# Kernel tuning notes

Measured on AMD Instinct MI355X. Metric: run time of the kernel, lower is better.

## Reference

```python
import jax, jax.numpy as jnp
import numpy as np
from jax import lax

N_FRAMES = 256

def _conv(x, w, b):
    # NCHW conv, stride 3 on mel axis (matches MOSNet CNN that collapses mels 81->27->9->3->1)
    y = lax.conv_general_dilated(x, w, window_strides=(1, 3),
                                 padding=((1, 1), (1, 1)),
                                 dimension_numbers=('NCHW', 'OIHW', 'NCHW'))
    return jax.nn.relu(y + b[None, :, None, None])

def _lstm(x, Wih, Whh, bih, bhh, reverse=False):
    # x: [T, B, D] -> hs: [T, B, H]; PyTorch gate order i, f, g, o
    Bsz, H = x.shape[1], Whh.shape[1]
    bias = bih + bhh
    def step(carry, xt):
        h, c = carry
        z = xt @ Wih.T + h @ Whh.T + bias
        i, f, g, o = jnp.split(z, 4, axis=-1)
        c = jax.nn.sigmoid(f) * c + jax.nn.sigmoid(i) * jnp.tanh(g)
        h = jax.nn.sigmoid(o) * jnp.tanh(c)
        return (h, c), h
    init = (jnp.zeros((Bsz, H), x.dtype), jnp.zeros((Bsz, H), x.dtype))
    _, hs = lax.scan(step, init, x, reverse=reverse)
    return hs

def setup_inputs():
    key = jax.random.key(0)
    ks = jax.random.split(key, 24)
    B, T, M = 16, 4096, 81
    chans = [1, 16, 32, 64, 128]
    H = 128
    FC_IN = 2 * H * N_FRAMES  # 65536
    FC_H = 128
    s = 0.05
    inp = {'audio': jax.random.normal(ks[0], (B, T, M), jnp.float32),
           'sample_lengths': jnp.full((B,), T, dtype=jnp.int32)}
    for li in range(4):
        inp['w%d' % li] = jax.random.normal(ks[1 + 2 * li], (chans[li + 1], chans[li], 3, 3), jnp.float32) * s
        inp['b%d' % li] = jnp.zeros((chans[li + 1],), jnp.float32)
    D = chans[-1]
    for d, off in (('f', 9), ('b', 13)):
        inp['Wih_' + d] = jax.random.normal(ks[off], (4 * H, D), jnp.float32) * s
        inp['Whh_' + d] = jax.random.normal(ks[off + 1], (4 * H, H), jnp.float32) * s
        inp['bih_' + d] = jnp.zeros((4 * H,), jnp.float32)
        inp['bhh_' + d] = jnp.zeros((4 * H,), jnp.float32)
    inp['fc1_w'] = jax.random.normal(ks[17], (FC_H, FC_IN), jnp.float32) * 0.005
    inp['fc1_b'] = jnp.zeros((FC_H,), jnp.float32)
    inp['fs_w'] = jax.random.normal(ks[18], (1, FC_H), jnp.float32) * s
    inp['fs_b'] = jnp.zeros((1,), jnp.float32)
    return inp

def reference(audio, w0, b0, w1, b1, w2, b2, w3, b3,
              Wih_f, Whh_f, bih_f, bhh_f, Wih_b, Whh_b, bih_b, bhh_b,
              fc1_w, fc1_b, fs_w, fs_b, sample_lengths):
    B, T, M = audio.shape
    F = T // N_FRAMES  # all lengths == T, multiple of N_FRAMES -> all frames full
    x = audio.reshape(B * F, 1, N_FRAMES, M)   # [BF, 1, nf, mels]
    for w, b in ((w0, b0), (w1, b1), (w2, b2), (w3, b3)):
        x = _conv(x, w, b)                      # mel axis 81->27->9->3->1
    x = x[..., 0].transpose(2, 0, 1)            # [nf, BF, C]
    h_f = _lstm(x, Wih_f, Whh_f, bih_f, bhh_f)
    h_b = _lstm(x, Wih_b, Whh_b, bih_b, bhh_b, reverse=True)
    h = jnp.concatenate([h_f, h_b], axis=-1).transpose(1, 0, 2)  # [BF, nf, 2H]
    flat = h.reshape(B * F, -1)                 # time-major flatten, matches view(1,-1)
    z = jax.nn.relu(flat @ fc1_w.T + fc1_b)     # dropout is identity at inference
    score = jax.nn.sigmoid(z @ fs_w.T + fs_b) * 4.0 + 1.0  # mos range [1,5]
    frames = score.reshape(B, F)
    utt = frames.mean(axis=1)
    return utt, frames
```

## Files before the change

### kernel.cpp

```cpp
#include <hip/hip_runtime.h>
#include <hip/hip_fp16.h>

#define BF 256
#define TSTEPS 256

typedef _Float16 h8_t __attribute__((ext_vector_type(8)));
typedef _Float16 h4_t __attribute__((ext_vector_type(4)));
typedef float f4_t __attribute__((ext_vector_type(4)));

union H8 { uint4 u; h8_t v; };
union H4 { uint2 u; h4_t v; };
union U2H4 { uint2 u; __half h[4]; };

static __device__ __forceinline__ float sigmoidf_(float x) {
    return 1.f / (1.f + __expf(-x));
}
static __device__ __forceinline__ float tanhf_(float x) {
    return 1.f - 2.f / (__expf(2.f * x) + 1.f);
}

static __device__ __forceinline__ void pack_one(const float* __restrict__ src,
                                                __half* __restrict__ dst,
                                                int OC, int IC, int KS,
                                                int oc_str, int ic_str, int k_str, int i) {
    int grp = KS / 4;
    int j = i % grp;
    int oc = (i / grp) % OC;
    int g = (i / (grp * OC)) & 3;
    int chunk = i / (grp * OC * 4);
    int CPK = IC / KS;
    int cc = chunk % CPK;
    int khw = chunk / CPK;
    int ic = cc * KS + g * grp + j;
    dst[i] = __float2half(src[(long)oc * oc_str + (long)ic * ic_str + khw * k_str]);
}

__global__ __launch_bounds__(256) void prep_k(
        const float* __restrict__ w0, const float* __restrict__ w1,
        const float* __restrict__ w2, const float* __restrict__ w3,
        const float* __restrict__ Wihf, const float* __restrict__ Wihb,
        const float* __restrict__ Whhf, const float* __restrict__ Whhb,
        float* __restrict__ w0t, __half* __restrict__ w1p,
        __half* __restrict__ w2p, __half* __restrict__ w3p,
        __half* __restrict__ wfp, __half* __restrict__ wbp,
        __half* __restrict__ whhfp, __half* __restrict__ whhbp) {
    int i = blockIdx.x * 256 + threadIdx.x;
    if (i < 144) { int oc = i / 9, rem = i % 9; w0t[rem * 16 + oc] = w0[i]; return; }
    i -= 144;
    if (i < 4608) { pack_one(w1, w1p, 32, 16, 16, 144, 9, 1, i); return; }
    i -= 4608;
    if (i < 18432) { pack_one(w2, w2p, 64, 32, 32, 288, 9, 1, i); return; }
    i -= 18432;
    if (i < 73728) { pack_one(w3, w3p, 128, 64, 32, 576, 9, 1, i); return; }
    i -= 73728;
    if (i < 65536) { pack_one(Wihf, wfp, 512, 128, 32, 128, 1, 0, i); return; }
    i -= 65536;
    if (i < 65536) { pack_one(Wihb, wbp, 512, 128, 32, 128, 1, 0, i); return; }
    i -= 65536;
    if (i < 65536) { pack_one(Whhf, whhfp, 512, 128, 32, 128, 1, 0, i); return; }
    i -= 65536;
    if (i < 65536) { pack_one(Whhb, whhbp, 512, 128, 32, 128, 1, 0, i); return; }
}

__global__ void pack_wf16(const float* __restrict__ src, __half* __restrict__ dst,
                          int OC, int IC, int KS,
                          int oc_str, int ic_str, int k_str, int total) {
    int i = blockIdx.x * 256 + threadIdx.x;
    if (i >= total) return;
    pack_one(src, dst, OC, IC, KS, oc_str, ic_str, k_str, i);
}

__global__ __launch_bounds__(256) void conv0_k(const float* __restrict__ in,
                                               const float* __restrict__ wT,
                                               const float* __restrict__ bias,
                                               __half* __restrict__ out) {
    __shared__ float wsm[9][16];
    __shared__ float bs[16];
    int tid = threadIdx.x;
    if (tid < 144) wsm[tid / 16][tid % 16] = wT[tid];
    if (tid < 16) bs[tid] = bias[tid];
    __syncthreads();
    int gid = blockIdx.x * 256 + tid;
    int ow = gid % 27;
    int t = (gid / 27) % 256;
    int bf = gid / (27 * 256);
    float acc[16];
#pragma unroll
    for (int o = 0; o < 16; o++) acc[o] = bs[o];
    int iw0 = ow * 3 - 1;
#pragma unroll
    for (int kh = 0; kh < 3; kh++) {
        int tt = t + kh - 1;
        if ((unsigned)tt >= 256u) continue;
        const float* ip = in + ((long)bf * 256 + tt) * 81;
#pragma unroll
        for (int kw = 0; kw < 3; kw++) {
            int iw = iw0 + kw;
            if ((unsigned)iw >= 81u) continue;
            float x = ip[iw];
#pragma unroll
            for (int o = 0; o < 16; o++) acc[o] += x * wsm[kh * 3 + kw][o];
        }
    }
    __half2* op = (__half2*)(out + (long)gid * 16);
#pragma unroll
    for (int o = 0; o < 8; o++)
        op[o] = __floats2half2_rn(fmaxf(acc[2 * o], 0.f), fmaxf(acc[2 * o + 1], 0.f));
}

template<int IC, int OC, int WIN, int WOUT, int KS>
__global__ __launch_bounds__(256) void convM_k(const __half* __restrict__ in,
                                               const __half* __restrict__ wp,
                                               const float* __restrict__ bias,
                                               __half* __restrict__ out) {
    constexpr int NT = OC / 16;
    constexpr int CPK = IC / KS;
    constexpr int NCHUNK = 9 * CPK;
    constexpr int GRP = KS / 4;
    int tid = threadIdx.x;
    int lane = tid & 63;
    int wv = tid >> 6;
    int l15 = lane & 15;
    int g = lane >> 4;
    int m = blockIdx.x * 64 + wv * 16 + l15;
    int ow = m % WOUT;
    int t = (m / WOUT) % 256;
    int bf = m / (WOUT * 256);

    f4_t acc[NT];
#pragma unroll
    for (int nt = 0; nt < NT; nt++)
#pragma unroll
        for (int r = 0; r < 4; r++) acc[nt][r] = 0.f;

#pragma unroll
    for (int chunk = 0; chunk < NCHUNK; chunk++) {
        int khw = chunk / CPK, cc = chunk % CPK;
        int kh = khw / 3;
        int kw = khw - kh * 3;
        int tt = t + kh - 1;
        int iw = ow * 3 + kw - 1;
        bool ok = ((unsigned)tt < 256u) && ((unsigned)iw < (unsigned)WIN);
        long aoff = ok ? (((long)(bf * 256 + tt) * WIN + iw) * IC + cc * KS + g * GRP) : 0;
        if constexpr (KS == 32) {
            H8 af;
            af.u = *(const uint4*)(in + aoff);
            if (!ok) af.u = make_uint4(0u, 0u, 0u, 0u);
#pragma unroll
            for (int nt = 0; nt < NT; nt++) {
                H8 bf8;
                bf8.u = *(const uint4*)(wp + ((long)(chunk * 4 + g) * OC + nt * 16 + l15) * GRP);
                acc[nt] = __builtin_amdgcn_mfma_f32_16x16x32_f16(af.v, bf8.v, acc[nt], 0, 0, 0);
            }
        } else {
            H4 af;
            af.u = *(const uint2*)(in + aoff);
            if (!ok) af.u = make_uint2(0u, 0u);
#pragma unroll
            for (int nt = 0; nt < NT; nt++) {
                H4 bf4;
                bf4.u = *(const uint2*)(wp + ((long)(chunk * 4 + g) * OC + nt * 16 + l15) * GRP);
                acc[nt] = __builtin_amdgcn_mfma_f32_16x16x16f16(af.v, bf4.v, acc[nt], 0, 0, 0);
            }
        }
    }
    int orow = blockIdx.x * 64 + wv * 16 + g * 4;
#pragma unroll
    for (int nt = 0; nt < NT; nt++) {
        int oc = nt * 16 + l15;
        float b = bias[oc];
#pragma unroll
        for (int r = 0; r < 4; r++) {
            float v = fmaxf(acc[nt][r] + b, 0.f);
            out[(long)(orow + r) * OC + oc] = __float2half(v);
        }
    }
}

__global__ __launch_bounds__(256) void gates_k(const __half* __restrict__ X,
                                               const __half* __restrict__ wpf,
                                               const __half* __restrict__ wpb,
                                               const float* __restrict__ bf1,
                                               const float* __restrict__ bf2,
                                               const float* __restrict__ bb1,
                                               const float* __restrict__ bb2,
                                               __half* __restrict__ Gf,
                                               __half* __restrict__ Gb) {
    int dir = blockIdx.z;
    const __half* wp = dir ? wpb : wpf;
    const float* b1 = dir ? bb1 : bf1;
    const float* b2 = dir ? bb2 : bf2;
    __half* G = dir ? Gb : Gf;
    int tid = threadIdx.x;
    int lane = tid & 63;
    int wv = tid >> 6;
    int l15 = lane & 15;
    int g = lane >> 4;
    long r0 = (long)blockIdx.x * 128 + wv * 32;
    int n0 = blockIdx.y * 128;

    f4_t acc[2][8];
#pragma unroll
    for (int s = 0; s < 2; s++)
#pragma unroll
        for (int nt = 0; nt < 8; nt++)
#pragma unroll
            for (int r = 0; r < 4; r++) acc[s][nt][r] = 0.f;

#pragma unroll
    for (int chunk = 0; chunk < 4; chunk++) {
        H8 a0, a1;
        a0.u = *(const uint4*)(X + (r0 + l15) * 128 + chunk * 32 + g * 8);
        a1.u = *(const uint4*)(X + (r0 + 16 + l15) * 128 + chunk * 32 + g * 8);
#pragma unroll
        for (int nt = 0; nt < 8; nt++) {
            H8 bw;
            bw.u = *(const uint4*)(wp + ((long)(chunk * 4 + g) * 512 + n0 + nt * 16 + l15) * 8);
            acc[0][nt] = __builtin_amdgcn_mfma_f32_16x16x32_f16(a0.v, bw.v, acc[0][nt], 0, 0, 0);
            acc[1][nt] = __builtin_amdgcn_mfma_f32_16x16x32_f16(a1.v, bw.v, acc[1][nt], 0, 0, 0);
        }
    }
    int b = (int)(r0 >> 8);
#pragma unroll
    for (int nt = 0; nt < 8; nt++) {
        int col = n0 + nt * 16 + l15;
        float bias = b1[col] + b2[col];
        long base = ((long)b * 512 + col) * 256;
#pragma unroll
        for (int s = 0; s < 2; s++) {
            int tb = (int)(r0 & 255) + s * 16 + g * 4;
            U2H4 pk;
            if (!dir) {
#pragma unroll
                for (int r = 0; r < 4; r++) pk.h[r] = __float2half(acc[s][nt][r] + bias);
                *(uint2*)(G + base + tb) = pk.u;
            } else {
#pragma unroll
                for (int r = 0; r < 4; r++) pk.h[3 - r] = __float2half(acc[s][nt][r] + bias);
                *(uint2*)(G + base + (252 - tb)) = pk.u;
            }
        }
    }
}

__global__ __launch_bounds__(512, 2) void lstm_k(const __half* __restrict__ Gf,
                                                 const __half* __restrict__ Gb,
                                                 const __half* __restrict__ whhfp,
                                                 const __half* __restrict__ whhbp,
                                                 __half* __restrict__ flat) {
    int bid = blockIdx.x;
    int dir = bid >> 7;
    int b0 = (bid & 127) * 2;
    const __half* G = dir ? Gb : Gf;
    const __half* wp = dir ? whhbp : whhfp;
    int tid = threadIdx.x;
    int w = tid >> 6;
    int lane = tid & 63;
    int l15 = lane & 15;
    int g2 = lane >> 4;
    int chn = l15 >> 3;
    int r = l15 & 3;
    int bit2 = (l15 >> 2) & 1;
    int ua = w * 16 + g2 * 4 + r;
    bool wrt = bit2 && ((r & 1) == 0);

    H8 afr[4][4];
#pragma unroll
    for (int k = 0; k < 4; k++) {
        int gate = k * 128 + w * 16 + l15;
#pragma unroll
        for (int c = 0; c < 4; c++)
            afr[k][c].u = *(const uint4*)(wp + ((long)((c * 4 + g2) * 512 + gate)) * 8);
    }

    __shared__ __align__(16) __half hbuf[2][2][128];
    if (tid < 256) hbuf[0][tid >> 7][tid & 127] = __float2half(0.f);
    __syncthreads();

    const __half* gb0 = G + (((long)(b0 + chn) * 512) + bit2 * 256 + ua) * 256;
    const __half* gb1 = gb0 + 128 * 256;

    float cst = 0.f;
    float ma = bit2 ? 2.f : 1.f;
    float mb = bit2 ? 2.f : 1.f;
    float cb = bit2 ? -1.f : 0.f;
    const f4_t zero4 = {0.f, 0.f, 0.f, 0.f};

    H8 gc0, gc1, gn0, gn1;
    gc0.u = *(const uint4*)(gb0);
    gc1.u = *(const uint4*)(gb1);
    long fbase = (long)(b0 + chn) * 65536 + dir * 128 + ua;

    for (int to = 0; to < 32; to++) {
        if (to < 31) {
            gn0.u = *(const uint4*)(gb0 + (to + 1) * 8);
            gn1.u = *(const uint4*)(gb1 + (to + 1) * 8);
        }
#pragma unroll
        for (int ti = 0; ti < 8; ti++) {
            int s = to * 8 + ti;
            int p = s & 1;
            H8 bfr[4];
#pragma unroll
            for (int c = 0; c < 4; c++)
                bfr[c].u = *(const uint4*)(&hbuf[p][chn][c * 32 + g2 * 8]);

            f4_t acc[4];
#pragma unroll
            for (int k = 0; k < 4; k++)
                acc[k] = __builtin_amdgcn_mfma_f32_16x16x32_f16(afr[k][0].v, bfr[0].v,
                                                                zero4, 0, 0, 0);
#pragma unroll
            for (int c = 1; c < 4; c++)
#pragma unroll
                for (int k = 0; k < 4; k++)
                    acc[k] = __builtin_amdgcn_mfma_f32_16x16x32_f16(afr[k][c].v, bfr[c].v,
                                                                    acc[k], 0, 0, 0);
            f4_t aA, aB;
#pragma unroll
            for (int e = 0; e < 4; e++) {
                aA[e] = bit2 ? acc[2][e] : acc[0][e];
                aB[e] = bit2 ? acc[3][e] : acc[1][e];
            }
            float loA = (r & 1) ? aA[1] : aA[0];
            float hiA = (r & 1) ? aA[3] : aA[2];
            float eA = (r & 2) ? hiA : loA;
            float loB = (r & 1) ? aB[1] : aB[0];
            float hiB = (r & 1) ? aB[3] : aB[2];
            float eB = (r & 2) ? hiB : loB;

            float za = eA + (float)gc0.v[ti];
            float zb = eB + (float)gc1.v[ti];
            float sa = sigmoidf_(ma * za);
            float fa = sa * mb + cb;
            float sb = sigmoidf_(zb);
            float grecv = __shfl_xor(fa, 4, 64);
            float cn = sb * cst + fa * grecv;
            cst = cn;
            float tc = tanhf_(cn);
            float tcr = __shfl_xor(tc, 4, 64);
            float h = sb * tcr;
            float hp = __shfl_xor(h, 1, 64);
            if (wrt) {
                __half2 h2 = __floats2half2_rn(h, hp);
                int ts = dir ? (255 - s) : s;
                *(__half2*)(&hbuf[p ^ 1][chn][ua]) = h2;
                *(__half2*)(flat + fbase + (long)ts * 256) = h2;
            }
            __syncthreads();
        }
        gc0 = gn0;
        gc1 = gn1;
    }
}

__global__ __launch_bounds__(256) void fc1m_k(const __half* __restrict__ flat,
                                              const __half* __restrict__ wp,
                                              float* __restrict__ z) {
    int tid = threadIdx.x;
    int lane = tid & 63;
    int wv = tid >> 6;
    int l15 = lane & 15;
    int g = lane >> 4;
    int m0 = blockIdx.x * 64 + wv * 16;
    long k0 = (long)blockIdx.y * 1024;

    f4_t acc[8];
#pragma unroll
    for (int nt = 0; nt < 8; nt++)
#pragma unroll
        for (int r = 0; r < 4; r++) acc[nt][r] = 0.f;

    for (int c = 0; c < 32; c++) {
        long chunk = (k0 >> 5) + c;
        H8 af;
        af.u = *(const uint4*)(flat + (long)(m0 + l15) * 65536 + k0 + c * 32 + g * 8);
#pragma unroll
        for (int nt = 0; nt < 8; nt++) {
            H8 bw;
            bw.u = *(const uint4*)(wp + ((chunk * 4 + g) * 128 + nt * 16 + l15) * 8);
            acc[nt] = __builtin_amdgcn_mfma_f32_16x16x32_f16(af.v, bw.v, acc[nt], 0, 0, 0);
        }
    }
#pragma unroll
    for (int nt = 0; nt < 8; nt++)
#pragma unroll
        for (int r = 0; r < 4; r++)
            atomicAdd(&z[(m0 + g * 4 + r) * 128 + nt * 16 + l15], acc[nt][r]);
}

__global__ void zero_k(float* __restrict__ p, int n) {
    int i = blockIdx.x * 256 + threadIdx.x;
    if (i < n) p[i] = 0.f;
}

__global__ __launch_bounds__(256) void head_k(const float* __restrict__ z,
                                              const float* __restrict__ b1,
                                              const float* __restrict__ fsw,
                                              const float* __restrict__ fsb,
                                              float* __restrict__ out) {
    __shared__ float sf[256];
    int r = threadIdx.x;
    float acc = fsb[0];
#pragma unroll
    for (int j4 = 0; j4 < 32; j4++) {
        float4 zv = *(const float4*)&z[r * 128 + j4 * 4];
        float4 bv = *(const float4*)&b1[j4 * 4];
        float4 wv = *(const float4*)&fsw[j4 * 4];
        acc += fmaxf(zv.x + bv.x, 0.f) * wv.x;
        acc += fmaxf(zv.y + bv.y, 0.f) * wv.y;
        acc += fmaxf(zv.z + bv.z, 0.f) * wv.z;
        acc += fmaxf(zv.w + bv.w, 0.f) * wv.w;
    }
    float val = sigmoidf_(acc) * 4.f + 1.f;
    out[16 + r] = val;
    sf[r] = val;
    __syncthreads();
    if (r < 16) {
        float m = 0.f;
#pragma unroll
        for (int f = 0; f < 16; f++) m += sf[r * 16 + f];
        out[r] = m * (1.f / 16.f);
    }
}

extern "C" void kernel_launch(void* const* d_in, const int* in_sizes, int n_in,
                              void* d_out, int out_size, void* d_ws, size_t ws_size,
                              hipStream_t stream) {
    const float* audio = (const float*)d_in[0];
    const float* w0 = (const float*)d_in[2];
    const float* b0 = (const float*)d_in[3];
    const float* w1 = (const float*)d_in[4];
    const float* b1 = (const float*)d_in[5];
    const float* w2 = (const float*)d_in[6];
    const float* b2 = (const float*)d_in[7];
    const float* w3 = (const float*)d_in[8];
    const float* b3 = (const float*)d_in[9];
    const float* Wih_f = (const float*)d_in[10];
    const float* Whh_f = (const float*)d_in[11];
    const float* bih_f = (const float*)d_in[12];
    const float* bhh_f = (const float*)d_in[13];
    const float* Wih_b = (const float*)d_in[14];
    const float* Whh_b = (const float*)d_in[15];
    const float* bih_b = (const float*)d_in[16];
    const float* bhh_b = (const float*)d_in[17];
    const float* fc1_w = (const float*)d_in[18];
    const float* fc1_b = (const float*)d_in[19];
    const float* fs_w = (const float*)d_in[20];
    const float* fs_b = (const float*)d_in[21];
    float* out = (float*)d_out;

    char* ws = (char*)d_ws;
    __half* Gf    = (__half*)(ws);
    __half* out1  = (__half*)(ws);
    __half* fc1p  = (__half*)(ws);
    __half* Gb    = (__half*)(ws + 67108864);
    __half* flat16= (__half*)(ws + 134217728);
    __half* out0  = (__half*)(ws + 134217728);
    __half* X     = (__half*)(ws + 201326592);
    __half* out2  = (__half*)(ws + 218103808);
    char* rd = ws + 243269632;
    float*  w0t   = (float*)(rd);
    __half* w1p   = (__half*)(rd + 1024);
    __half* w2p   = (__half*)(rd + 10240);
    __half* w3p   = (__half*)(rd + 47104);
    __half* wfp   = (__half*)(rd + 194560);
    __half* wbp   = (__half*)(rd + 325632);
    __half* whhfp = (__half*)(rd + 456704);
    __half* whhbp = (__half*)(rd + 587776);
    float*  zbuf  = (float*)(rd + 718848);

    prep_k<<<1403, 256, 0, stream>>>(w0, w1, w2, w3, Wih_f, Wih_b, Whh_f, Whh_b,
                                     w0t, w1p, w2p, w3p, wfp, wbp, whhfp, whhbp);

    conv0_k<<<6912, 256, 0, stream>>>(audio, w0t, b0, out0);
    convM_k<16, 32, 27, 9, 16><<<9216, 256, 0, stream>>>(out0, w1p, b1, out1);
    convM_k<32, 64, 9, 3, 32><<<3072, 256, 0, stream>>>(out1, w2p, b2, out2);
    convM_k<64, 128, 3, 1, 32><<<1024, 256, 0, stream>>>(out2, w3p, b3, X);

    gates_k<<<dim3(512, 4, 2), 256, 0, stream>>>(X, wfp, wbp, bih_f, bhh_f,
                                                 bih_b, bhh_b, Gf, Gb);

    lstm_k<<<256, 512, 0, stream>>>(Gf, Gb, whhfp, whhbp, flat16);

    pack_wf16<<<32768, 256, 0, stream>>>(fc1_w, fc1p, 128, 65536, 32, 65536, 1, 0, 8388608);
    zero_k<<<128, 256, 0, stream>>>(zbuf, 256 * 128);
    fc1m_k<<<dim3(4, 64), 256, 0, stream>>>(flat16, fc1p, zbuf);
    head_k<<<1, 256, 0, stream>>>(zbuf, fc1_b, fs_w, fs_b, out);
}
```

Baseline: 535.5 us.

## Stage LSTM hidden states in LDS history ring and flush coalesced every 16 steps

The recurrent LSTM kernel now keeps the hidden state for 16 consecutive steps in a padded shared-memory ring. Before, it used a two-slot ping-pong buffer. The per-step scattered half2 global stores to the flattened output are removed. Instead, every 16 steps all threads copy the buffered rows out with coalesced 16-byte stores. The aim is to take global-store traffic off the serial recurrence's critical path. In exchange, the gate-input loads are no longer prefetched one block ahead, and there is an extra barrier per 16-step group.

Measured after the change: 553.9 us. +3.4%, slower.

```diff
diff --git a/kernel.cpp b/kernel.cpp
--- a/kernel.cpp
+++ b/kernel.cpp
@@ -273,37 +273,34 @@
             afr[k][c].u = *(const uint4*)(wp + ((long)((c * 4 + g2) * 512 + gate)) * 8);
     }
 
-    __shared__ __align__(16) __half hbuf[2][2][128];
-    if (tid < 256) hbuf[0][tid >> 7][tid & 127] = __float2half(0.f);
+    __shared__ __align__(16) __half hist[16][320];
+    if (tid < 160) { hist[15][tid] = __float2half(0.f);
+                     hist[15][160 + tid] = __float2half(0.f); }
     __syncthreads();
 
-    const __half* gb0 = G + (((long)(b0 + chn) * 512) + bit2 * 256 + ua) * 256;
-    const __half* gb1 = gb0 + 128 * 256;
+    const __half* gp0 = G + (((long)(b0 + chn) * 512) + bit2 * 256 + ua) * 256;
+    const __half* gp1 = gp0 + 128 * 256;
 
     float cst = 0.f;
     float ma = bit2 ? 2.f : 1.f;
-    float mb = bit2 ? 2.f : 1.f;
+    float mb = ma;
     float cb = bit2 ? -1.f : 0.f;
     const f4_t zero4 = {0.f, 0.f, 0.f, 0.f};
 
-    H8 gc0, gc1, gn0, gn1;
-    gc0.u = *(const uint4*)(gb0);
-    gc1.u = *(const uint4*)(gb1);
-    long fbase = (long)(b0 + chn) * 65536 + dir * 128 + ua;
-
-    for (int to = 0; to < 32; to++) {
-        if (to < 31) {
-            gn0.u = *(const uint4*)(gb0 + (to + 1) * 8);
-            gn1.u = *(const uint4*)(gb1 + (to + 1) * 8);
-        }
-#pragma unroll
-        for (int ti = 0; ti < 8; ti++) {
-            int s = to * 8 + ti;
-            int p = s & 1;
+    for (int go = 0; go < 16; go++) {
+        H8 gA0, gA1, gB0, gB1;
+        gA0.u = *(const uint4*)(gp0 + go * 16);
+        gA1.u = *(const uint4*)(gp0 + go * 16 + 8);
+        gB0.u = *(const uint4*)(gp1 + go * 16);
+        gB1.u = *(const uint4*)(gp1 + go * 16 + 8);
+
+#pragma unroll
+        for (int j = 0; j < 16; j++) {
+            int rs = (j + 15) & 15;
             H8 bfr[4];
 #pragma unroll
             for (int c = 0; c < 4; c++)
-                bfr[c].u = *(const uint4*)(&hbuf[p][chn][c * 32 + g2 * 8]);
+                bfr[c].u = *(const uint4*)(&hist[rs][chn * 160 + c * 32 + g2 * 8]);
 
             f4_t acc[4];
 #pragma unroll
@@ -329,8 +326,10 @@
             float hiB = (r & 1) ? aB[3] : aB[2];
             float eB = (r & 2) ? hiB : loB;
 
-            float za = eA + (float)gc0.v[ti];
-            float zb = eB + (float)gc1.v[ti];
+            float ga = (float)((j < 8) ? gA0.v[j & 7] : gA1.v[j & 7]);
+            float gb = (float)((j < 8) ? gB0.v[j & 7] : gB1.v[j & 7]);
+            float za = eA + ga;
+            float zb = eB + gb;
             float sa = sigmoidf_(ma * za);
             float fa = sa * mb + cb;
             float sb = sigmoidf_(zb);
@@ -341,16 +340,21 @@
             float tcr = __shfl_xor(tc, 4, 64);
             float h = sb * tcr;
             float hp = __shfl_xor(h, 1, 64);
-            if (wrt) {
-                __half2 h2 = __floats2half2_rn(h, hp);
-                int ts = dir ? (255 - s) : s;
-                *(__half2*)(&hbuf[p ^ 1][chn][ua]) = h2;
-                *(__half2*)(flat + fbase + (long)ts * 256) = h2;
-            }
+            if (wrt)
+                *(__half2*)(&hist[j][chn * 160 + ua]) = __floats2half2_rn(h, hp);
             __syncthreads();
         }
-        gc0 = gn0;
-        gc1 = gn1;
+
+        {
+            int fj = tid >> 5;
+            int fch = (tid >> 4) & 1;
+            int ck = tid & 15;
+            int s = go * 16 + fj;
+            int ts = dir ? (255 - s) : s;
+            uint4 v = *(const uint4*)(&hist[fj][fch * 160 + ck * 8]);
+            *(uint4*)(flat + (long)(b0 + fch) * 65536 + (long)ts * 256 + dir * 128 + ck * 8) = v;
+        }
+        __syncthreads();
     }
 }
 
```
